# Kernel optimization log

Measured on AMD Instinct MI355X. Metric: run time of the kernel, lower is better.

Reference implementation:

```python
import jax, jax.numpy as jnp
import numpy as np

DELTA = 0.1
LRELU_SLOPE = 0.01
BN_EPS = 1e-5


def ternarize(t, d):
    # {-1, 0, +1}: 0 where |t| < d, sign(t) otherwise (matches the torch where-chain)
    return jnp.where(jnp.abs(t) < d, 0.0, jnp.sign(t))


def ste_ternarize(t, d):
    # straight-through estimator, matching the torch .data-swap trick
    return t + jax.lax.stop_gradient(ternarize(t, d) - t)


def conv2d(x, w, stride, pad):
    return jax.lax.conv_general_dilated(
        x, w, (stride, stride), [(pad, pad), (pad, pad)],
        dimension_numbers=('NCHW', 'OIHW', 'NCHW'))


def batchnorm(x, gamma, beta, mean, var):
    inv = gamma / jnp.sqrt(var + BN_EPS)
    return x * inv[None, :, None, None] + (beta - mean * inv)[None, :, None, None]


def lrelu(x):
    return jnp.where(x > 0, x, LRELU_SLOPE * x)


def setup_inputs() -> dict:
    key = jax.random.key(0)
    ks = jax.random.split(key, 12)
    B, Cin, C, H, W = 16, 32, 64, 256, 256
    return {
        'x':      jax.random.normal(ks[0], (B, Cin, H, W), jnp.float32),
        'w11':    jax.random.normal(ks[1], (C, Cin, 3, 3), jnp.float32),
        'b11':    jax.random.normal(ks[2], (C,), jnp.float32),
        'w1':     jax.random.normal(ks[3], (C, Cin, 3, 3), jnp.float32),
        'b1':     jax.random.normal(ks[4], (C,), jnp.float32),
        'w2':     jax.random.normal(ks[5], (C, C, 3, 3), jnp.float32),
        'b2':     jax.random.normal(ks[6], (C,), jnp.float32),
        'gamma_p': jax.random.uniform(ks[7], (Cin,), jnp.float32),
        'beta_p':  jax.random.normal(ks[8], (Cin,), jnp.float32),
        'mean_p':  jax.random.normal(ks[9], (Cin,), jnp.float32),
        'var_p':   jnp.ones((Cin,), jnp.float32),
        'gamma1':  jax.random.uniform(ks[10], (C,), jnp.float32),
        'beta1':   jax.random.normal(ks[11], (C,), jnp.float32),
        'mean1':   jax.random.normal(jax.random.fold_in(key, 99), (C,), jnp.float32),
        'var1':    jnp.ones((C,), jnp.float32),
    }


def reference(x, w11, b11, w1, b1, w2, b2,
              gamma_p, beta_p, mean_p, var_p,
              gamma1, beta1, mean1, var1):
    # shortcut conv11 (stride 3); NOTE: torch mutates input.data in-place, so
    # the main branch below consumes the x already ternarized with d11.
    d11 = DELTA * jnp.max(jnp.abs(w11))
    x_t = ste_ternarize(x, d11)
    prev_mp = conv2d(x_t, ste_ternarize(w11, d11), 3, 1) \
        + ste_ternarize(b11, d11)[None, :, None, None]

    # main branch: pre_bn -> lrelu -> conv1 (stride 1) -> bn1 -> lrelu -> dropout(eval) -> conv2 (stride 3)
    out = lrelu(batchnorm(x_t, gamma_p, beta_p, mean_p, var_p))

    d1 = DELTA * jnp.max(jnp.abs(w1))
    out = conv2d(ste_ternarize(out, d1), ste_ternarize(w1, d1), 1, 1) \
        + ste_ternarize(b1, d1)[None, :, None, None]
    out = lrelu(batchnorm(out, gamma1, beta1, mean1, var1))
    # dropout: identity in eval mode

    d2 = DELTA * jnp.max(jnp.abs(w2))
    out = conv2d(ste_ternarize(out, d2), ste_ternarize(w2, d2), 3, 1) \
        + ste_ternarize(b2, d2)[None, :, None, None]

    return lrelu(out + prev_mp)  # [16, 64, 86, 86]
```

## Files before the change

### kernel.cpp

```cpp
#include <hip/hip_runtime.h>
#include <stdint.h>

#define B 16
#define CIN 32
#define C 64
#define H 256
#define W 256
#define OH 86
#define OW 86
#define PIX (OH*OW)

typedef int v4i __attribute__((ext_vector_type(4)));

#define OFF_D      0
#define OFF_MAPW   64
#define OFF_S1     256
#define OFF_SH1    512
#define OFF_B11    768
#define OFF_B1     1024
#define OFF_B2     1280
#define OFF_W11P   4096
#define OFF_W1P    24576
#define OFF_W2P    45056
#define OFF_XTP    262144
#define OFF_PREV   33816576
#define OFF_T2P    48963584

__device__ __forceinline__ int tern_i(float t, float d) {
    return (fabsf(t) < d) ? 0 : (t > 0.f ? 1 : -1);
}

__global__ void k_zero(unsigned* d) {
    if (threadIdx.x < 3) d[threadIdx.x] = 0u;
}

__global__ __launch_bounds__(256) void k_absmax(const float* w11, const float* w1,
                                                const float* w2, unsigned* dws) {
    __shared__ unsigned red[256];
    int b = blockIdx.x >> 4, sub = blockIdx.x & 15;
    const float* p = (b == 0) ? w11 : (b == 1) ? w1 : w2;
    int n = (b == 2) ? 36864 : 18432;
    int chunk = (n + 15) >> 4;
    int lo = sub * chunk, hi = min(lo + chunk, n);
    unsigned m = 0;
    for (int i = lo + threadIdx.x; i < hi; i += 256)
        m = max(m, __float_as_uint(fabsf(p[i])));
    red[threadIdx.x] = m; __syncthreads();
    for (int s = 128; s > 0; s >>= 1) {
        if (threadIdx.x < s) red[threadIdx.x] = max(red[threadIdx.x], red[threadIdx.x + s]);
        __syncthreads();
    }
    if (threadIdx.x == 0) atomicMax(&dws[b], red[0]);
}

__global__ __launch_bounds__(256) void k_prep(const float* w11, const float* w1, const float* w2,
                                              const float* b11, const float* b1, const float* b2,
                                              const float* gp, const float* bp, const float* mp, const float* vp,
                                              const float* g1, const float* be1, const float* me1, const float* v1,
                                              char* ws) {
    const unsigned* dw = (const unsigned*)(ws + OFF_D);
    float d11 = __fmul_rn(0.1f, __uint_as_float(dw[0]));
    float d1  = __fmul_rn(0.1f, __uint_as_float(dw[1]));
    float d2v = __fmul_rn(0.1f, __uint_as_float(dw[2]));
    int idx = blockIdx.x * 256 + threadIdx.x;
    if (idx < 4608) {
        int k = idx >> 6, co = idx & 63;
        int pos = k >> 3, g = k & 7;
        unsigned wd = 0;
        #pragma unroll
        for (int j = 0; j < 4; j++) {
            int tv = tern_i(w1[(co * 32 + g * 4 + j) * 9 + pos], d1);
            wd |= ((unsigned)(tv & 255)) << (8 * j);
        }
        ((int*)(ws + OFF_W1P))[idx] = (int)wd;
    } else if (idx < 9216) {
        int i2 = idx - 4608;
        int g = i2 & 7, c16 = (i2 >> 3) & 15, hcot = (i2 >> 7) & 3, pos = i2 >> 9;
        int co = hcot * 16 + c16;
        unsigned wd = 0;
        #pragma unroll
        for (int j = 0; j < 4; j++) {
            int tv = tern_i(w11[(co * 32 + g * 4 + j) * 9 + pos], d11);
            wd |= ((unsigned)(tv & 255)) << (8 * j);
        }
        ((int*)(ws + OFF_W11P))[i2] = (int)wd;
    } else if (idx < 18432) {
        int i2 = idx - 9216;
        int g = i2 & 15, c16 = (i2 >> 4) & 15, hcot = (i2 >> 8) & 3, pos = i2 >> 10;
        int co = hcot * 16 + c16;
        unsigned wd = 0;
        #pragma unroll
        for (int j = 0; j < 4; j++) {
            int tv = tern_i(w2[(co * 64 + g * 4 + j) * 9 + pos], d2v);
            wd |= ((unsigned)(tv & 255)) << (8 * j);
        }
        ((int*)(ws + OFF_W2P))[i2] = (int)wd;
    } else {
        int i = idx - 18432;
        if (i < 64) {
            ((int*)(ws + OFF_B11))[i] = tern_i(b11[i], d11);
        } else if (i < 128) {
            ((int*)(ws + OFF_B1))[i - 64] = tern_i(b1[i - 64], d1);
        } else if (i < 192) {
            ((int*)(ws + OFF_B2))[i - 128] = tern_i(b2[i - 128], d2v);
        } else if (i < 216) {
            int j = i - 192;
            int g = j / 3, s = j % 3;
            float v = (float)(s - 1);
            unsigned wd = 0;
            #pragma unroll
            for (int jj = 0; jj < 4; jj++) {
                int c = g * 4 + jj;
                float inv = __fdiv_rn(gp[c], __fsqrt_rn(__fadd_rn(vp[c], 1e-5f)));
                float sh  = __fsub_rn(bp[c], __fmul_rn(mp[c], inv));
                float z   = __fadd_rn(__fmul_rn(v, inv), sh);
                z = (z > 0.f) ? z : __fmul_rn(0.01f, z);
                wd |= ((unsigned)(tern_i(z, d1) & 255)) << (8 * jj);
            }
            ((int*)(ws + OFF_MAPW))[j] = (int)wd;
        } else if (i < 280) {
            int c = i - 216;
            float inv = __fdiv_rn(g1[c], __fsqrt_rn(__fadd_rn(v1[c], 1e-5f)));
            ((float*)(ws + OFF_S1))[c]  = inv;
            ((float*)(ws + OFF_SH1))[c] = __fsub_rn(be1[c], __fmul_rn(me1[c], inv));
        }
    }
}

__global__ __launch_bounds__(256) void k_tern_x(const float* __restrict__ x,
                                                char* __restrict__ ws) {
    float d11 = __fmul_rn(0.1f, __uint_as_float(((const unsigned*)(ws + OFF_D))[0]));
    int idx = blockIdx.x * 256 + threadIdx.x;
    int pix = idx & 65535, n = idx >> 16;
    const float* xp = x + ((size_t)n * CIN << 16) + pix;
    int w[8];
    #pragma unroll
    for (int g = 0; g < 8; ++g) {
        unsigned wd = 0;
        #pragma unroll
        for (int j = 0; j < 4; ++j) {
            float v = xp[(size_t)(g * 4 + j) << 16];
            wd |= ((unsigned)(tern_i(v, d11) & 255)) << (8 * j);
        }
        w[g] = (int)wd;
    }
    int4* o = (int4*)(ws + OFF_XTP) + ((size_t)idx * 2);
    o[0] = make_int4(w[0], w[1], w[2], w[3]);
    o[1] = make_int4(w[4], w[5], w[6], w[7]);
}

__global__ __launch_bounds__(256) void k_conv11(const char* __restrict__ ws) {
    int tid = threadIdx.x, bid = blockIdx.x;
    int tile = bid % 116, n = bid / 116;
    int c16 = tid & 15, q = (tid >> 4) & 3, wv = tid >> 6;
    int h = wv & 1, ph = wv >> 1;
    const int* w11q = (const int*)(ws + OFF_W11P);
    const int* xtp = (const int*)(ws + OFF_XTP) + (size_t)n * 524288;
    const int* b11i = (const int*)(ws + OFF_B11);
    int bco[2] = { b11i[h * 32 + c16], b11i[h * 32 + 16 + c16] };
    short* prev = (short*)(ws + OFF_PREV) + (size_t)n * C * PIX;
    int pbase = tile * 64;
    #pragma unroll
    for (int pgi = 0; pgi < 2; ++pgi) {
        int pg = ph * 2 + pgi;
        int pA = pbase + pg * 16 + c16;
        int oh = pA / 86, ow = pA - oh * 86;
        v4i a[5];
        #pragma unroll
        for (int c = 0; c < 5; ++c) {
            int pos = 2 * c + (q >> 1);
            v4i z = {0, 0, 0, 0};
            if (pos < 9) {
                int kh = pos / 3, kw = pos - kh * 3;
                int ih = oh * 3 - 1 + kh, iw = ow * 3 - 1 + kw;
                if (pA < PIX && (unsigned)ih < H && (unsigned)iw < W)
                    z = *(const v4i*)&xtp[(ih * 256 + iw) * 8 + (q & 1) * 4];
            }
            a[c] = z;
        }
        #pragma unroll
        for (int cot = 0; cot < 2; ++cot) {
            int hc = h * 2 + cot;
            v4i acc = {0, 0, 0, 0};
            #pragma unroll
            for (int c = 0; c < 5; ++c) {
                int pos = 2 * c + (q >> 1);
                v4i b = {0, 0, 0, 0};
                if (pos < 9)
                    b = *(const v4i*)&w11q[((pos * 4 + hc) * 16 + c16) * 8 + (q & 1) * 4];
                acc = __builtin_amdgcn_mfma_i32_16x16x64_i8(a[c], b, acc, 0, 0, 0);
            }
            int co = h * 32 + cot * 16 + c16;
            int p0 = pbase + pg * 16 + q * 4;
            #pragma unroll
            for (int i = 0; i < 4; ++i) {
                int p = p0 + i;
                if (p < PIX) prev[co * PIX + p] = (short)(acc[i] + bco[cot]);
            }
        }
    }
}

__global__ __launch_bounds__(256, 2) void k_conv1(const char* __restrict__ ws) {
    __shared__ int tin[2592];
    __shared__ int mapw[24];
    int tid = threadIdx.x;
    int bid = blockIdx.x;
    int twx = bid & 15, twy = (bid >> 4) & 15, n = bid >> 8;
    if (tid < 24) mapw[tid] = ((const int*)(ws + OFF_MAPW))[tid];
    __syncthreads();
    const int* xtp = (const int*)(ws + OFF_XTP) + (size_t)n * 524288;
    int Y0 = twy * 16, X0 = twx * 16;
    int y0 = Y0 - 1, x0 = X0 - 1;
    for (int i = tid; i < 648; i += 256) {
        int r = i / 36, cq = i % 36;
        int p = cq >> 1, gb = (cq & 1) * 4;
        int gy = y0 + r, gx = x0 + p;
        int mw[4] = {0, 0, 0, 0};
        if ((unsigned)gy < H && (unsigned)gx < W) {
            int4 v = *(const int4*)&xtp[(gy * 256 + gx) * 8 + gb];
            #pragma unroll
            for (int j = 0; j < 4; ++j) {
                unsigned t = (j == 0) ? (unsigned)v.x : (j == 1) ? (unsigned)v.y
                           : (j == 2) ? (unsigned)v.z : (unsigned)v.w;
                unsigned nb = (t & 0x80808080u) >> 7;
                unsigned pb = (t & 0x01010101u) & ~nb;
                unsigned nm = nb * 0xFFu, pm = pb * 0xFFu;
                unsigned zm = ~(nm | pm);
                int g = gb + j;
                unsigned Wn = (unsigned)mapw[g * 3 + 0];
                unsigned W0 = (unsigned)mapw[g * 3 + 1];
                unsigned Wp = (unsigned)mapw[g * 3 + 2];
                mw[j] = (int)((Wn & nm) | (W0 & zm) | (Wp & pm));
            }
        }
        *(int4*)&tin[(r * 18 + p) * 8 + gb] = make_int4(mw[0], mw[1], mw[2], mw[3]);
    }
    int c16 = tid & 15, q = (tid >> 4) & 3;
    const int* w1p = (const int*)(ws + OFF_W1P);
    int bw[5][4][4];
    #pragma unroll
    for (int c = 0; c < 5; ++c) {
        int pos = 2 * c + (q >> 1);
        #pragma unroll
        for (int ct = 0; ct < 4; ++ct)
            #pragma unroll
            for (int j = 0; j < 4; ++j)
                bw[c][ct][j] = (pos < 9) ? w1p[(pos * 8 + (q & 1) * 4 + j) * 64 + ct * 16 + c16] : 0;
    }
    const int* b1i = (const int*)(ws + OFF_B1);
    const float* s1 = (const float*)(ws + OFF_S1);
    const float* sh1 = (const float*)(ws + OFF_SH1);
    float d2v = __fmul_rn(0.1f, __uint_as_float(((const unsigned*)(ws + OFF_D))[2]));
    int bco[4]; float sco[4], shco[4];
    #pragma unroll
    for (int ct = 0; ct < 4; ++ct) {
        int co = ct * 16 + c16;
        bco[ct] = b1i[co]; sco[ct] = s1[co]; shco[ct] = sh1[co];
    }
    __syncthreads();
    int wv = tid >> 6;
    char* t2base = (char*)ws + OFF_T2P + ((size_t)n << 22);
    #pragma unroll
    for (int tt = 0; tt < 4; ++tt) {
        int t = wv * 4 + tt;
        v4i a[5];
        #pragma unroll
        for (int c = 0; c < 5; ++c) {
            int pos = 2 * c + (q >> 1);
            if (pos < 9) {
                int kh = pos / 3, kw = pos - kh * 3;
                a[c] = *(const v4i*)&tin[((t + kh) * 18 + (c16 + kw)) * 8 + (q & 1) * 4];
            } else {
                v4i z = {0, 0, 0, 0};
                a[c] = z;
            }
        }
        #pragma unroll
        for (int ct = 0; ct < 4; ++ct) {
            v4i acc = {0, 0, 0, 0};
            #pragma unroll
            for (int c = 0; c < 5; ++c) {
                v4i b = {bw[c][ct][0], bw[c][ct][1], bw[c][ct][2], bw[c][ct][3]};
                acc = __builtin_amdgcn_mfma_i32_16x16x64_i8(a[c], b, acc, 0, 0, 0);
            }
            int y = Y0 + t;
            int gw = ct * 4 + (c16 >> 2);
            #pragma unroll
            for (int i = 0; i < 4; ++i) {
                int xg = X0 + q * 4 + i;
                int vi = acc[i] + bco[ct];
                float z = __fadd_rn(__fmul_rn((float)vi, sco[ct]), shco[ct]);
                z = (z > 0.f) ? z : __fmul_rn(0.01f, z);
                signed char tv = (fabsf(z) < d2v) ? 0 : (z > 0.f ? 1 : -1);
                t2base[(((size_t)((y << 8) + xg)) << 6) + (gw << 2) + (c16 & 3)] = tv;
            }
        }
    }
}

__global__ __launch_bounds__(256) void k_conv2(const char* __restrict__ ws,
                                               float* __restrict__ out) {
    int tid = threadIdx.x, bid = blockIdx.x;
    int tile = bid % 116, n = bid / 116;
    int c16 = tid & 15, q = (tid >> 4) & 3, wv = tid >> 6;
    int h = wv & 1, ph = wv >> 1;
    const int* w2q = (const int*)(ws + OFF_W2P);
    const char* t2 = (const char*)ws + OFF_T2P + ((size_t)n << 22);
    const int* b2i = (const int*)(ws + OFF_B2);
    int bco[2] = { b2i[h * 32 + c16], b2i[h * 32 + 16 + c16] };
    const short* prev = (const short*)(ws + OFF_PREV) + (size_t)n * C * PIX;
    float* outn = out + (size_t)n * C * PIX;
    int pbase = tile * 64;
    #pragma unroll
    for (int pgi = 0; pgi < 2; ++pgi) {
        int pg = ph * 2 + pgi;
        int pA = pbase + pg * 16 + c16;
        int oh = pA / 86, ow = pA - oh * 86;
        v4i a[9];
        #pragma unroll
        for (int pos = 0; pos < 9; ++pos) {
            int kh = pos / 3, kw = pos - kh * 3;
            int ih = oh * 3 - 1 + kh, iw = ow * 3 - 1 + kw;
            v4i z = {0, 0, 0, 0};
            if (pA < PIX && (unsigned)ih < H && (unsigned)iw < W)
                z = *(const v4i*)(t2 + (((size_t)((ih << 8) + iw)) << 6) + (q << 4));
            a[pos] = z;
        }
        #pragma unroll
        for (int cot = 0; cot < 2; ++cot) {
            int hc = h * 2 + cot;
            v4i acc = {0, 0, 0, 0};
            #pragma unroll
            for (int pos = 0; pos < 9; ++pos) {
                v4i b = *(const v4i*)&w2q[((pos * 4 + hc) * 16 + c16) * 16 + q * 4];
                acc = __builtin_amdgcn_mfma_i32_16x16x64_i8(a[pos], b, acc, 0, 0, 0);
            }
            int co = h * 32 + cot * 16 + c16;
            int p0 = pbase + pg * 16 + q * 4;
            #pragma unroll
            for (int i = 0; i < 4; ++i) {
                int p = p0 + i;
                if (p < PIX) {
                    int v = acc[i] + bco[cot] + (int)prev[co * PIX + p];
                    float z2 = (float)v;
                    outn[(size_t)co * PIX + p] = (z2 > 0.f) ? z2 : __fmul_rn(0.01f, z2);
                }
            }
        }
    }
}

extern "C" void kernel_launch(void* const* d_in, const int* in_sizes, int n_in,
                              void* d_out, int out_size, void* d_ws, size_t ws_size,
                              hipStream_t stream) {
    const float* x    = (const float*)d_in[0];
    const float* w11  = (const float*)d_in[1];
    const float* b11  = (const float*)d_in[2];
    const float* w1   = (const float*)d_in[3];
    const float* b1   = (const float*)d_in[4];
    const float* w2   = (const float*)d_in[5];
    const float* b2   = (const float*)d_in[6];
    const float* gp   = (const float*)d_in[7];
    const float* bp   = (const float*)d_in[8];
    const float* mp   = (const float*)d_in[9];
    const float* vp   = (const float*)d_in[10];
    const float* g1   = (const float*)d_in[11];
    const float* be1  = (const float*)d_in[12];
    const float* me1  = (const float*)d_in[13];
    const float* v1   = (const float*)d_in[14];
    char* ws = (char*)d_ws;
    float* out = (float*)d_out;

    k_zero<<<1, 64, 0, stream>>>((unsigned*)(ws + OFF_D));
    k_absmax<<<48, 256, 0, stream>>>(w11, w1, w2, (unsigned*)(ws + OFF_D));
    k_prep<<<74, 256, 0, stream>>>(w11, w1, w2, b11, b1, b2,
                                   gp, bp, mp, vp, g1, be1, me1, v1, ws);
    k_tern_x<<<4096, 256, 0, stream>>>(x, ws);
    k_conv11<<<116 * B, 256, 0, stream>>>(ws);
    k_conv1<<<4096, 256, 0, stream>>>(ws);
    k_conv2<<<116 * B, 256, 0, stream>>>(ws, out);
}
```

Measured before the change: 152.5 us.

## Fuse shortcut, conv1 and strided conv2 into one tiled kernel via LDS

Replaces the three separate conv kernels with one kernel per 8x8 output tile. The kernel computes the shortcut conv, then the 24x24 conv1 region needed by the stride-3 conv2 into shared memory, then conv2 plus residual and activation. The BN/LReLU input map is precomputed in the ternarize pass with a swizzled layout, and weight packing is reordered for the new MFMA access pattern. This removes the global round trips of the full-resolution intermediate and the shortcut buffer. In exchange it adds large shared-memory use, barriers and lower occupancy.

```diff
diff --git a/kernel.cpp b/kernel.cpp
--- a/kernel.cpp
+++ b/kernel.cpp
@@ -19,12 +19,11 @@
 #define OFF_B11    768
 #define OFF_B1     1024
 #define OFF_B2     1280
-#define OFF_W11P   4096
-#define OFF_W1P    24576
-#define OFF_W2P    45056
+#define OFF_W11R   4096
+#define OFF_W1R    24576
+#define OFF_W2R    45056
 #define OFF_XTP    262144
-#define OFF_PREV   33816576
-#define OFF_T2P    48963584
+#define OFF_XMAP   33816576
 
 __device__ __forceinline__ int tern_i(float t, float d) {
     return (fabsf(t) < d) ? 0 : (t > 0.f ? 1 : -1);
@@ -64,37 +63,43 @@
     float d2v = __fmul_rn(0.1f, __uint_as_float(dw[2]));
     int idx = blockIdx.x * 256 + threadIdx.x;
     if (idx < 4608) {
-        int k = idx >> 6, co = idx & 63;
-        int pos = k >> 3, g = k & 7;
+        int j = idx & 3, c16 = (idx >> 2) & 15, cot = (idx >> 6) & 1;
+        int h = (idx >> 7) & 1, q1 = (idx >> 8) & 1, pos = idx >> 9;
+        int co = h * 32 + cot * 16 + c16;
         unsigned wd = 0;
         #pragma unroll
-        for (int j = 0; j < 4; j++) {
-            int tv = tern_i(w1[(co * 32 + g * 4 + j) * 9 + pos], d1);
-            wd |= ((unsigned)(tv & 255)) << (8 * j);
-        }
-        ((int*)(ws + OFF_W1P))[idx] = (int)wd;
+        for (int jj = 0; jj < 4; jj++) {
+            int ci = q1 * 16 + j * 4 + jj;
+            int tv = tern_i(w1[(co * 32 + ci) * 9 + pos], d1);
+            wd |= ((unsigned)(tv & 255)) << (8 * jj);
+        }
+        ((int*)(ws + OFF_W1R))[idx] = (int)wd;
     } else if (idx < 9216) {
         int i2 = idx - 4608;
-        int g = i2 & 7, c16 = (i2 >> 3) & 15, hcot = (i2 >> 7) & 3, pos = i2 >> 9;
-        int co = hcot * 16 + c16;
+        int j = i2 & 3, c16 = (i2 >> 2) & 15, cot = (i2 >> 6) & 3;
+        int q1 = (i2 >> 8) & 1, pos = i2 >> 9;
+        int co = cot * 16 + c16;
         unsigned wd = 0;
         #pragma unroll
-        for (int j = 0; j < 4; j++) {
-            int tv = tern_i(w11[(co * 32 + g * 4 + j) * 9 + pos], d11);
-            wd |= ((unsigned)(tv & 255)) << (8 * j);
-        }
-        ((int*)(ws + OFF_W11P))[i2] = (int)wd;
+        for (int jj = 0; jj < 4; jj++) {
+            int ci = q1 * 16 + j * 4 + jj;
+            int tv = tern_i(w11[(co * 32 + ci) * 9 + pos], d11);
+            wd |= ((unsigned)(tv & 255)) << (8 * jj);
+        }
+        ((int*)(ws + OFF_W11R))[i2] = (int)wd;
     } else if (idx < 18432) {
         int i2 = idx - 9216;
-        int g = i2 & 15, c16 = (i2 >> 4) & 15, hcot = (i2 >> 8) & 3, pos = i2 >> 10;
-        int co = hcot * 16 + c16;
+        int j = i2 & 3, c16 = (i2 >> 2) & 15, cot = (i2 >> 6) & 3;
+        int q1 = (i2 >> 8) & 1, h = (i2 >> 9) & 1, pos = i2 >> 10;
+        int co = cot * 16 + c16;
         unsigned wd = 0;
         #pragma unroll
-        for (int j = 0; j < 4; j++) {
-            int tv = tern_i(w2[(co * 64 + g * 4 + j) * 9 + pos], d2v);
-            wd |= ((unsigned)(tv & 255)) << (8 * j);
-        }
-        ((int*)(ws + OFF_W2P))[i2] = (int)wd;
+        for (int jj = 0; jj < 4; jj++) {
+            int ci = h * 32 + q1 * 16 + j * 4 + jj;
+            int tv = tern_i(w2[(co * 64 + ci) * 9 + pos], d2v);
+            wd |= ((unsigned)(tv & 255)) << (8 * jj);
+        }
+        ((int*)(ws + OFF_W2R))[i2] = (int)wd;
     } else {
         int i = idx - 18432;
         if (i < 64) {
@@ -130,222 +135,225 @@
 __global__ __launch_bounds__(256) void k_tern_x(const float* __restrict__ x,
                                                 char* __restrict__ ws) {
     float d11 = __fmul_rn(0.1f, __uint_as_float(((const unsigned*)(ws + OFF_D))[0]));
+    const int* mapw = (const int*)(ws + OFF_MAPW);
     int idx = blockIdx.x * 256 + threadIdx.x;
     int pix = idx & 65535, n = idx >> 16;
+    int gx = pix & 255;
     const float* xp = x + ((size_t)n * CIN << 16) + pix;
-    int w[8];
+    int rw[8], mw[8];
     #pragma unroll
     for (int g = 0; g < 8; ++g) {
-        unsigned wd = 0;
+        unsigned r = 0, m = 0;
         #pragma unroll
         for (int j = 0; j < 4; ++j) {
             float v = xp[(size_t)(g * 4 + j) << 16];
-            wd |= ((unsigned)(tern_i(v, d11) & 255)) << (8 * j);
-        }
-        w[g] = (int)wd;
-    }
-    int4* o = (int4*)(ws + OFF_XTP) + ((size_t)idx * 2);
-    o[0] = make_int4(w[0], w[1], w[2], w[3]);
-    o[1] = make_int4(w[4], w[5], w[6], w[7]);
-}
-
-__global__ __launch_bounds__(256) void k_conv11(const char* __restrict__ ws) {
+            int tv = tern_i(v, d11);
+            r |= ((unsigned)(tv & 255)) << (8 * j);
+            m |= (((unsigned)mapw[g * 3 + tv + 1] >> (8 * j)) & 255u) << (8 * j);
+        }
+        rw[g] = (int)r; mw[g] = (int)m;
+    }
+    int4* o1 = (int4*)(ws + OFF_XTP) + ((size_t)idx * 2);
+    o1[0] = make_int4(rw[0], rw[1], rw[2], rw[3]);
+    o1[1] = make_int4(rw[4], rw[5], rw[6], rw[7]);
+    int f = (gx & 1) ^ ((gx >> 2) & 1);
+    int4* o2 = (int4*)(ws + OFF_XMAP) + ((size_t)idx * 2);
+    o2[f]     = make_int4(mw[0], mw[1], mw[2], mw[3]);
+    o2[f ^ 1] = make_int4(mw[4], mw[5], mw[6], mw[7]);
+}
+
+#define T2S 12
+__global__ __launch_bounds__(256) void k_net(const char* __restrict__ ws,
+                                             float* __restrict__ out) {
+    __shared__ int mapL[676 * 8];
+    __shared__ int t2L[576 * T2S];
     int tid = threadIdx.x, bid = blockIdx.x;
-    int tile = bid % 116, n = bid / 116;
+    int tx = bid % 11; int tt = bid / 11; int ty = tt % 11; int n = tt / 11;
+    int OH0 = ty * 8, OW0 = tx * 8;
+    int Y0 = OH0 * 3 - 2, X0 = OW0 * 3 - 2;
     int c16 = tid & 15, q = (tid >> 4) & 3, wv = tid >> 6;
-    int h = wv & 1, ph = wv >> 1;
-    const int* w11q = (const int*)(ws + OFF_W11P);
-    const int* xtp = (const int*)(ws + OFF_XTP) + (size_t)n * 524288;
-    const int* b11i = (const int*)(ws + OFF_B11);
-    int bco[2] = { b11i[h * 32 + c16], b11i[h * 32 + 16 + c16] };
-    short* prev = (short*)(ws + OFF_PREV) + (size_t)n * C * PIX;
-    int pbase = tile * 64;
-    #pragma unroll
-    for (int pgi = 0; pgi < 2; ++pgi) {
-        int pg = ph * 2 + pgi;
-        int pA = pbase + pg * 16 + c16;
-        int oh = pA / 86, ow = pA - oh * 86;
+    int q1 = q & 1, qh = q >> 1;
+    const int* xmapn = (const int*)(ws + OFF_XMAP + ((size_t)n << 21));
+    const int* xtpn  = (const int*)(ws + OFF_XTP  + ((size_t)n << 21));
+
+    for (int i = tid; i < 1352; i += 256) {
+        int pix = i >> 1, hf = i & 1;
+        int my = pix / 26, mx = pix - my * 26;
+        int gy = Y0 + my, gxv = X0 + mx;
+        int4 v = make_int4(0, 0, 0, 0);
+        if ((unsigned)gy < H && (unsigned)gxv < W)
+            v = *(const int4*)&xmapn[(gy * 256 + gxv) * 8 + hf * 4];
+        *(int4*)&mapL[pix * 8 + hf * 4] = v;
+    }
+
+    int o = wv * 16 + c16;
+    int oh8 = o >> 3, ow8 = o & 7;
+    int gOH = OH0 + oh8, gOW = OW0 + ow8;
+    bool pvalid = (gOH < OH) && (gOW < OW);
+    const int* w11r = (const int*)(ws + OFF_W11R);
+    v4i acc11[4];
+    {
         v4i a[5];
         #pragma unroll
         for (int c = 0; c < 5; ++c) {
-            int pos = 2 * c + (q >> 1);
+            int pos = 2 * c + qh;
             v4i z = {0, 0, 0, 0};
             if (pos < 9) {
                 int kh = pos / 3, kw = pos - kh * 3;
-                int ih = oh * 3 - 1 + kh, iw = ow * 3 - 1 + kw;
-                if (pA < PIX && (unsigned)ih < H && (unsigned)iw < W)
-                    z = *(const v4i*)&xtp[(ih * 256 + iw) * 8 + (q & 1) * 4];
+                int ih = gOH * 3 - 1 + kh, iw = gOW * 3 - 1 + kw;
+                if (pvalid && (unsigned)ih < H && (unsigned)iw < W)
+                    z = *(const v4i*)&xtpn[(ih * 256 + iw) * 8 + q1 * 4];
             }
             a[c] = z;
         }
         #pragma unroll
-        for (int cot = 0; cot < 2; ++cot) {
-            int hc = h * 2 + cot;
+        for (int cot = 0; cot < 4; ++cot) {
             v4i acc = {0, 0, 0, 0};
             #pragma unroll
             for (int c = 0; c < 5; ++c) {
-                int pos = 2 * c + (q >> 1);
+                int pos = 2 * c + qh;
                 v4i b = {0, 0, 0, 0};
                 if (pos < 9)
-                    b = *(const v4i*)&w11q[((pos * 4 + hc) * 16 + c16) * 8 + (q & 1) * 4];
+                    b = *(const v4i*)&w11r[((pos * 2 + q1) * 4 + cot) * 64 + c16 * 4];
                 acc = __builtin_amdgcn_mfma_i32_16x16x64_i8(a[c], b, acc, 0, 0, 0);
             }
-            int co = h * 32 + cot * 16 + c16;
-            int p0 = pbase + pg * 16 + q * 4;
-            #pragma unroll
-            for (int i = 0; i < 4; ++i) {
-                int p = p0 + i;
-                if (p < PIX) prev[co * PIX + p] = (short)(acc[i] + bco[cot]);
-            }
-        }
-    }
-}
-
-__global__ __launch_bounds__(256, 2) void k_conv1(const char* __restrict__ ws) {
-    __shared__ int tin[2592];
-    __shared__ int mapw[24];
-    int tid = threadIdx.x;
-    int bid = blockIdx.x;
-    int twx = bid & 15, twy = (bid >> 4) & 15, n = bid >> 8;
-    if (tid < 24) mapw[tid] = ((const int*)(ws + OFF_MAPW))[tid];
+            acc11[cot] = acc;
+        }
+    }
     __syncthreads();
-    const int* xtp = (const int*)(ws + OFF_XTP) + (size_t)n * 524288;
-    int Y0 = twy * 16, X0 = twx * 16;
-    int y0 = Y0 - 1, x0 = X0 - 1;
-    for (int i = tid; i < 648; i += 256) {
-        int r = i / 36, cq = i % 36;
-        int p = cq >> 1, gb = (cq & 1) * 4;
-        int gy = y0 + r, gx = x0 + p;
-        int mw[4] = {0, 0, 0, 0};
-        if ((unsigned)gy < H && (unsigned)gx < W) {
-            int4 v = *(const int4*)&xtp[(gy * 256 + gx) * 8 + gb];
-            #pragma unroll
-            for (int j = 0; j < 4; ++j) {
-                unsigned t = (j == 0) ? (unsigned)v.x : (j == 1) ? (unsigned)v.y
-                           : (j == 2) ? (unsigned)v.z : (unsigned)v.w;
-                unsigned nb = (t & 0x80808080u) >> 7;
-                unsigned pb = (t & 0x01010101u) & ~nb;
-                unsigned nm = nb * 0xFFu, pm = pb * 0xFFu;
-                unsigned zm = ~(nm | pm);
-                int g = gb + j;
-                unsigned Wn = (unsigned)mapw[g * 3 + 0];
-                unsigned W0 = (unsigned)mapw[g * 3 + 1];
-                unsigned Wp = (unsigned)mapw[g * 3 + 2];
-                mw[j] = (int)((Wn & nm) | (W0 & zm) | (Wp & pm));
-            }
-        }
-        *(int4*)&tin[(r * 18 + p) * 8 + gb] = make_int4(mw[0], mw[1], mw[2], mw[3]);
-    }
-    int c16 = tid & 15, q = (tid >> 4) & 3;
-    const int* w1p = (const int*)(ws + OFF_W1P);
-    int bw[5][4][4];
-    #pragma unroll
-    for (int c = 0; c < 5; ++c) {
-        int pos = 2 * c + (q >> 1);
-        #pragma unroll
-        for (int ct = 0; ct < 4; ++ct)
-            #pragma unroll
-            for (int j = 0; j < 4; ++j)
-                bw[c][ct][j] = (pos < 9) ? w1p[(pos * 8 + (q & 1) * 4 + j) * 64 + ct * 16 + c16] : 0;
-    }
+
+    const int* w1r = (const int*)(ws + OFF_W1R);
+    const int* w2r = (const int*)(ws + OFF_W2R);
     const int* b1i = (const int*)(ws + OFF_B1);
     const float* s1 = (const float*)(ws + OFF_S1);
     const float* sh1 = (const float*)(ws + OFF_SH1);
     float d2v = __fmul_rn(0.1f, __uint_as_float(((const unsigned*)(ws + OFF_D))[2]));
-    int bco[4]; float sco[4], shco[4];
+    v4i acc2[4];
     #pragma unroll
-    for (int ct = 0; ct < 4; ++ct) {
-        int co = ct * 16 + c16;
-        bco[ct] = b1i[co]; sco[ct] = s1[co]; shco[ct] = sh1[co];
-    }
-    __syncthreads();
-    int wv = tid >> 6;
-    char* t2base = (char*)ws + OFF_T2P + ((size_t)n << 22);
-    #pragma unroll
-    for (int tt = 0; tt < 4; ++tt) {
-        int t = wv * 4 + tt;
-        v4i a[5];
+    for (int cot = 0; cot < 4; ++cot) { v4i z = {0,0,0,0}; acc2[cot] = z; }
+
+    #pragma unroll 1
+    for (int h = 0; h < 2; ++h) {
+        v4i bw1[5][2];
+        int b1c[2]; float s1c[2], sh1c[2];
+        #pragma unroll
+        for (int cot = 0; cot < 2; ++cot) {
+            int co = h * 32 + cot * 16 + c16;
+            b1c[cot] = b1i[co]; s1c[cot] = s1[co]; sh1c[cot] = sh1[co];
+        }
         #pragma unroll
         for (int c = 0; c < 5; ++c) {
-            int pos = 2 * c + (q >> 1);
-            if (pos < 9) {
-                int kh = pos / 3, kw = pos - kh * 3;
-                a[c] = *(const v4i*)&tin[((t + kh) * 18 + (c16 + kw)) * 8 + (q & 1) * 4];
+            int pos = 2 * c + qh;
+            #pragma unroll
+            for (int cot = 0; cot < 2; ++cot) {
+                v4i z = {0, 0, 0, 0};
+                if (pos < 9)
+                    z = *(const v4i*)&w1r[(((pos * 2 + q1) * 2 + h) * 2 + cot) * 64 + c16 * 4];
+                bw1[c][cot] = z;
+            }
+        }
+        #pragma unroll 1
+        for (int pg = 0; pg < 9; ++pg) {
+            int pbase = (wv * 9 + pg) * 16;
+            int fp = pbase + c16;
+            int iy = fp / 24, ix = fp - iy * 24;
+            v4i a[5];
+            #pragma unroll
+            for (int c = 0; c < 5; ++c) {
+                int pos = 2 * c + qh;
+                v4i z = {0, 0, 0, 0};
+                if (pos < 9) {
+                    int kh = pos / 3, kw = pos - kh * 3;
+                    int my = iy + kh, mx = ix + kw;
+                    int gxl = X0 + mx;
+                    int hb = q1 ^ ((gxl & 1) ^ ((gxl >> 2) & 1));
+                    z = *(const v4i*)&mapL[(my * 26 + mx) * 8 + hb * 4];
+                }
+                a[c] = z;
+            }
+            int pwr = pbase + q * 4 + (c16 & 3);
+            int wy = pwr / 24, wx = pwr - wy * 24;
+            bool wok = ((unsigned)(Y0 + 1 + wy) < H) && ((unsigned)(X0 + 1 + wx) < W);
+            #pragma unroll
+            for (int cot = 0; cot < 2; ++cot) {
+                v4i acc = {0, 0, 0, 0};
+                #pragma unroll
+                for (int c = 0; c < 5; ++c)
+                    acc = __builtin_amdgcn_mfma_i32_16x16x64_i8(a[c], bw1[c][cot], acc, 0, 0, 0);
+                unsigned wcol = 0;
+                #pragma unroll
+                for (int i = 0; i < 4; ++i) {
+                    int vi = acc[i] + b1c[cot];
+                    float z = __fadd_rn(__fmul_rn((float)vi, s1c[cot]), sh1c[cot]);
+                    z = (z > 0.f) ? z : __fmul_rn(0.01f, z);
+                    int tv = (fabsf(z) < d2v) ? 0 : (z > 0.f ? 1 : -1);
+                    wcol |= ((unsigned)(tv & 255)) << (8 * i);
+                }
+                unsigned y1 = (unsigned)__shfl_xor((int)wcol, 1);
+                unsigned z1 = ((c16 & 1) == 0)
+                            ? __builtin_amdgcn_perm(y1, wcol, 0x06020400u)
+                            : __builtin_amdgcn_perm(y1, wcol, 0x03070105u);
+                unsigned y2 = (unsigned)__shfl_xor((int)z1, 2);
+                unsigned r  = ((c16 & 2) == 0)
+                            ? __builtin_amdgcn_perm(y2, z1, 0x05040100u)
+                            : __builtin_amdgcn_perm(y2, z1, 0x03020706u);
+                t2L[pwr * T2S + cot * 4 + (c16 >> 2)] = wok ? (int)r : 0;
+            }
+        }
+        __syncthreads();
+        {
+            v4i a2[5];
+            #pragma unroll
+            for (int c = 0; c < 5; ++c) {
+                int pos = 2 * c + qh;
+                v4i z = {0, 0, 0, 0};
+                if (pos < 9) {
+                    int kh = pos / 3, kw = pos - kh * 3;
+                    int p2 = (oh8 * 3 + kh) * 24 + (ow8 * 3 + kw);
+                    z = *(const v4i*)&t2L[p2 * T2S + q1 * 4];
+                }
+                a2[c] = z;
+            }
+            #pragma unroll
+            for (int cot = 0; cot < 4; ++cot) {
+                v4i acc = acc2[cot];
+                #pragma unroll
+                for (int c = 0; c < 5; ++c) {
+                    int pos = 2 * c + qh;
+                    v4i b = {0, 0, 0, 0};
+                    if (pos < 9)
+                        b = *(const v4i*)&w2r[((((pos * 2 + h) * 2 + q1) * 4 + cot)) * 64 + c16 * 4];
+                    acc = __builtin_amdgcn_mfma_i32_16x16x64_i8(a2[c], b, acc, 0, 0, 0);
+                }
+                acc2[cot] = acc;
+            }
+        }
+        __syncthreads();
+    }
+
+    const int* b2i = (const int*)(ws + OFF_B2);
+    const int* b11i = (const int*)(ws + OFF_B11);
+    int pt0 = wv * 16 + q * 4;
+    int ohh = OH0 + (pt0 >> 3);
+    int oww = OW0 + (pt0 & 7);
+    if (ohh < OH) {
+        #pragma unroll
+        for (int cot = 0; cot < 4; ++cot) {
+            int co = cot * 16 + c16;
+            int bc = b2i[co] + b11i[co];
+            float f[4];
+            #pragma unroll
+            for (int i = 0; i < 4; ++i) {
+                float z = (float)(acc2[cot][i] + acc11[cot][i] + bc);
+                f[i] = (z > 0.f) ? z : __fmul_rn(0.01f, z);
+            }
+            float* op = out + ((size_t)(n * 64 + co)) * PIX + ohh * OW + oww;
+            if (oww + 3 < OW) {
+                *(float4*)op = make_float4(f[0], f[1], f[2], f[3]);
             } else {
-                v4i z = {0, 0, 0, 0};
-                a[c] = z;
-            }
-        }
-        #pragma unroll
-        for (int ct = 0; ct < 4; ++ct) {
-            v4i acc = {0, 0, 0, 0};
-            #pragma unroll
-            for (int c = 0; c < 5; ++c) {
-                v4i b = {bw[c][ct][0], bw[c][ct][1], bw[c][ct][2], bw[c][ct][3]};
-                acc = __builtin_amdgcn_mfma_i32_16x16x64_i8(a[c], b, acc, 0, 0, 0);
-            }
-            int y = Y0 + t;
-            int gw = ct * 4 + (c16 >> 2);
-            #pragma unroll
-            for (int i = 0; i < 4; ++i) {
-                int xg = X0 + q * 4 + i;
-                int vi = acc[i] + bco[ct];
-                float z = __fadd_rn(__fmul_rn((float)vi, sco[ct]), shco[ct]);
-                z = (z > 0.f) ? z : __fmul_rn(0.01f, z);
-                signed char tv = (fabsf(z) < d2v) ? 0 : (z > 0.f ? 1 : -1);
-                t2base[(((size_t)((y << 8) + xg)) << 6) + (gw << 2) + (c16 & 3)] = tv;
-            }
-        }
-    }
-}
-
-__global__ __launch_bounds__(256) void k_conv2(const char* __restrict__ ws,
-                                               float* __restrict__ out) {
-    int tid = threadIdx.x, bid = blockIdx.x;
-    int tile = bid % 116, n = bid / 116;
-    int c16 = tid & 15, q = (tid >> 4) & 3, wv = tid >> 6;
-    int h = wv & 1, ph = wv >> 1;
-    const int* w2q = (const int*)(ws + OFF_W2P);
-    const char* t2 = (const char*)ws + OFF_T2P + ((size_t)n << 22);
-    const int* b2i = (const int*)(ws + OFF_B2);
-    int bco[2] = { b2i[h * 32 + c16], b2i[h * 32 + 16 + c16] };
-    const short* prev = (const short*)(ws + OFF_PREV) + (size_t)n * C * PIX;
-    float* outn = out + (size_t)n * C * PIX;
-    int pbase = tile * 64;
-    #pragma unroll
-    for (int pgi = 0; pgi < 2; ++pgi) {
-        int pg = ph * 2 + pgi;
-        int pA = pbase + pg * 16 + c16;
-        int oh = pA / 86, ow = pA - oh * 86;
-        v4i a[9];
-        #pragma unroll
-        for (int pos = 0; pos < 9; ++pos) {
-            int kh = pos / 3, kw = pos - kh * 3;
-            int ih = oh * 3 - 1 + kh, iw = ow * 3 - 1 + kw;
-            v4i z = {0, 0, 0, 0};
-            if (pA < PIX && (unsigned)ih < H && (unsigned)iw < W)
-                z = *(const v4i*)(t2 + (((size_t)((ih << 8) + iw)) << 6) + (q << 4));
-            a[pos] = z;
-        }
-        #pragma unroll
-        for (int cot = 0; cot < 2; ++cot) {
-            int hc = h * 2 + cot;
-            v4i acc = {0, 0, 0, 0};
-            #pragma unroll
-            for (int pos = 0; pos < 9; ++pos) {
-                v4i b = *(const v4i*)&w2q[((pos * 4 + hc) * 16 + c16) * 16 + q * 4];
-                acc = __builtin_amdgcn_mfma_i32_16x16x64_i8(a[pos], b, acc, 0, 0, 0);
-            }
-            int co = h * 32 + cot * 16 + c16;
-            int p0 = pbase + pg * 16 + q * 4;
-            #pragma unroll
-            for (int i = 0; i < 4; ++i) {
-                int p = p0 + i;
-                if (p < PIX) {
-                    int v = acc[i] + bco[cot] + (int)prev[co * PIX + p];
-                    float z2 = (float)v;
-                    outn[(size_t)co * PIX + p] = (z2 > 0.f) ? z2 : __fmul_rn(0.01f, z2);
-                }
+                #pragma unroll
+                for (int i = 0; i < 4; ++i)
+                    if (oww + i < OW) op[i] = f[i];
             }
         }
     }
@@ -377,7 +385,5 @@
     k_prep<<<74, 256, 0, stream>>>(w11, w1, w2, b11, b1, b2,
                                    gp, bp, mp, vp, g1, be1, me1, v1, ws);
     k_tern_x<<<4096, 256, 0, stream>>>(x, ws);
-    k_conv11<<<116 * B, 256, 0, stream>>>(ws);
-    k_conv1<<<4096, 256, 0, stream>>>(ws);
-    k_conv2<<<116 * B, 256, 0, stream>>>(ws, out);
-}
+    k_net<<<11 * 11 * B, 256, 0, stream>>>(ws, out);
+}
```

Result: no change. 149.7 us (-1.8%).
